# Performance work log

Hardware: AMD Instinct MI355X
Metric: run time of the kernel (lower is better)

Reference implementation:

```python
import jax, jax.numpy as jnp
import numpy as np

N_NODES, N_EDGES, D, N_RELS = 50000, 600000, 128, 460


def setup_inputs() -> dict:
    key = jax.random.key(0)
    ks = jax.random.split(key, 8)
    h = jax.random.normal(ks[0], (N_NODES, D), dtype=jnp.float32)
    emb_rel = jax.random.normal(ks[1], (N_RELS, D), dtype=jnp.float32)
    attn_fc_w = jax.random.normal(ks[2], (D, 3 * D), dtype=jnp.float32) * 0.05   # Linear(3D->D), weight [out,in]
    attn_fc2_w = jax.random.normal(ks[3], (1, D), dtype=jnp.float32) * 0.05     # Linear(D->1)
    loop_weight = jax.random.normal(ks[4], (D, D), dtype=jnp.float32) * 0.05
    edge_src = jax.random.randint(ks[5], (N_EDGES,), 0, N_NODES)
    edge_dst = jax.random.randint(ks[6], (N_EDGES,), 0, N_NODES)
    edge_type = jax.random.randint(ks[7], (N_EDGES,), 0, N_RELS)
    return {"h": h, "emb_rel": emb_rel, "attn_fc_w": attn_fc_w,
            "attn_fc2_w": attn_fc2_w, "loop_weight": loop_weight,
            "edge_src": edge_src, "edge_dst": edge_dst, "edge_type": edge_type}


def reference(h, emb_rel, attn_fc_w, attn_fc2_w, loop_weight, edge_src, edge_dst, edge_type):
    n = h.shape[0]
    # --- per-edge gather ---
    hs = h[edge_src]            # [E, D] src features (mailbox 'e_h')
    ht = h[edge_dst]            # [E, D]
    rel = emb_rel[edge_type]    # [E, D]
    # --- concat-MLP attention: leaky_relu(fc2(fc1([hs|ht|rel]))) ---
    z2 = jnp.concatenate([hs, ht, rel], axis=1)          # [E, 3D]
    a = z2 @ attn_fc_w.T                                  # [E, D]
    e = jax.nn.leaky_relu(a @ attn_fc2_w.T)               # [E, 1], slope 0.01 (torch default)
    # --- per-destination segment softmax ---
    m = jax.ops.segment_max(e, edge_dst, num_segments=n)  # [N, 1]
    m = jnp.where(jnp.isfinite(m), m, jnp.float32(0.0))   # empty nodes -> -inf; neutralize
    ex = jnp.exp(e - m[edge_dst])                         # [E, 1]
    den = jax.ops.segment_sum(ex, edge_dst, num_segments=n)
    alpha = ex / den[edge_dst]                            # [E, 1]
    # --- weighted scatter-sum of src features ---
    node_repr = jax.ops.segment_sum(alpha * hs, edge_dst, num_segments=n)  # [N, D]
    # --- self-loop ---
    node_repr = node_repr + h @ loop_weight
    return node_repr
```

## Files before the change

### kernel.cpp

```cpp
#include <hip/hip_runtime.h>

#define N_NODES 50000
#define N_EDGES 600000
#define D 128
#define N_RELS 460
#define CAP_LOG 6

typedef unsigned short u16;
typedef __attribute__((ext_vector_type(8))) short bf16x8;
typedef __attribute__((ext_vector_type(4))) float f32x4;

enum : int {
    OFF_W      = 0,
    OFF_S1     = 384,
    OFF_S2     = 50384,
    OFF_S3     = 100384,
    OFF_COUNTS = 100864,
    OFF_CSR    = 900864,
    OFF_HB     = 4100864,
};

#define NODE_WAVES   12500
#define REL_WAVES    115
#define SCORE_BLOCKS 3154
#define GEMM_BLOCKS  782
#define ZERO_BLOCKS  196
#define FILL_BLOCKS  586
#define WT_STRIDE    136

__device__ __forceinline__ u16 f2bf(float f) {
    unsigned u = __float_as_uint(f);
    unsigned r = u + 0x7FFFu + ((u >> 16) & 1u);
    return (u16)(r >> 16);
}

__global__ __launch_bounds__(256) void k_prep(
        const float* __restrict__ fc1, const float* __restrict__ fc2,
        const float* __restrict__ W, const float* __restrict__ h,
        float* __restrict__ w, int* __restrict__ counts,
        float* __restrict__ out) {
    __shared__ u16 Ws[D * WT_STRIDE];
    int t = threadIdx.x;
    if (blockIdx.x < GEMM_BLOCKS) {
        for (int i = t; i < (D * D) / 4; i += 256) {
            float4 v = ((const float4*)W)[i];
            int k  = i >> 5;
            int n0 = (i & 31) * 4;
            Ws[(n0 + 0) * WT_STRIDE + k] = f2bf(v.x);
            Ws[(n0 + 1) * WT_STRIDE + k] = f2bf(v.y);
            Ws[(n0 + 2) * WT_STRIDE + k] = f2bf(v.z);
            Ws[(n0 + 3) * WT_STRIDE + k] = f2bf(v.w);
        }
        __syncthreads();

        int wave = t >> 6, lane = t & 63;
        int quad = lane >> 4, m16 = lane & 15;
        int nbase = blockIdx.x * 64 + wave * 16;

        f32x4 acc[8];
        #pragma unroll
        for (int cg = 0; cg < 8; ++cg) acc[cg] = (f32x4){0.f, 0.f, 0.f, 0.f};

        int arow = nbase + m16;
        if (arow >= N_NODES) arow = N_NODES - 1;
        const float* aptr = h + (size_t)arow * D + quad * 8;

        #pragma unroll
        for (int k0 = 0; k0 < D; k0 += 32) {
            float4 a0 = *(const float4*)(aptr + k0);
            float4 a1 = *(const float4*)(aptr + k0 + 4);
            bf16x8 a;
            a[0] = (short)f2bf(a0.x); a[1] = (short)f2bf(a0.y);
            a[2] = (short)f2bf(a0.z); a[3] = (short)f2bf(a0.w);
            a[4] = (short)f2bf(a1.x); a[5] = (short)f2bf(a1.y);
            a[6] = (short)f2bf(a1.z); a[7] = (short)f2bf(a1.w);
            #pragma unroll
            for (int cg = 0; cg < 8; ++cg) {
                bf16x8 bb = *(const bf16x8*)(&Ws[(cg * 16 + m16) * WT_STRIDE + k0 + quad * 8]);
                acc[cg] = __builtin_amdgcn_mfma_f32_16x16x32_bf16(a, bb, acc[cg], 0, 0, 0);
            }
        }
        #pragma unroll
        for (int reg = 0; reg < 4; ++reg) {
            int row = nbase + quad * 4 + reg;
            if (row < N_NODES) {
                #pragma unroll
                for (int cg = 0; cg < 8; ++cg)
                    out[(size_t)row * D + cg * 16 + m16] = acc[cg][reg];
            }
        }
    } else if (blockIdx.x < GEMM_BLOCKS + ZERO_BLOCKS) {
        int base = ((blockIdx.x - GEMM_BLOCKS) * 256 + t) * 4;
        int i4 = ((blockIdx.x - GEMM_BLOCKS) * 256 + t);
        #pragma unroll
        for (int rep = 0; rep < 4; ++rep) {
            int idx = (i4 * 4 + rep);
            if (idx * 4 < N_NODES * 16)
                ((int4*)counts)[idx] = make_int4(0, 0, 0, 0);
        }
        (void)base;
    } else {
        for (int j = t; j < 3 * D; j += 256) {
            float acc = 0.f;
            for (int k = 0; k < D; ++k) acc += fc2[k] * fc1[k * 3 * D + j];
            w[j] = acc;
        }
    }
}

__global__ __launch_bounds__(256) void k_fused(
        const int* __restrict__ src, const int* __restrict__ dst,
        const int* __restrict__ typ, int* __restrict__ counts,
        unsigned* __restrict__ csr,
        const float* __restrict__ h, const float* __restrict__ emb_rel,
        const float* __restrict__ w,
        float* __restrict__ s1, float* __restrict__ s2, float* __restrict__ s3,
        u16* __restrict__ hb) {
    if (blockIdx.x < FILL_BLOCKS) {
        int i = blockIdx.x * blockDim.x + threadIdx.x;
        if (i >= N_EDGES / 4) return;
        int4 d4 = ((const int4*)dst)[i];
        int4 s4 = ((const int4*)src)[i];
        int4 t4 = ((const int4*)typ)[i];
        int sl0 = atomicAdd(&counts[d4.x << 4], 1);
        int sl1 = atomicAdd(&counts[d4.y << 4], 1);
        int sl2 = atomicAdd(&counts[d4.z << 4], 1);
        int sl3 = atomicAdd(&counts[d4.w << 4], 1);
        csr[(d4.x << CAP_LOG) + sl0] = (unsigned)s4.x | ((unsigned)t4.x << 16);
        csr[(d4.y << CAP_LOG) + sl1] = (unsigned)s4.y | ((unsigned)t4.y << 16);
        csr[(d4.z << CAP_LOG) + sl2] = (unsigned)s4.z | ((unsigned)t4.z << 16);
        csr[(d4.w << CAP_LOG) + sl3] = (unsigned)s4.w | ((unsigned)t4.w << 16);
    } else {
        int wv = ((blockIdx.x - FILL_BLOCKS) * blockDim.x + threadIdx.x) >> 6;
        int l  = threadIdx.x & 63;
        int sub = l >> 4;
        int q   = l & 15;
        if (wv < NODE_WAVES) {
            int r = wv * 4 + sub;
            const float* hp = h + (size_t)r * D + q * 8;
            float4 h0 = *(const float4*)hp;
            float4 h1 = *(const float4*)(hp + 4);
            uint4 pk;
            pk.x = (unsigned)f2bf(h0.x) | ((unsigned)f2bf(h0.y) << 16);
            pk.y = (unsigned)f2bf(h0.z) | ((unsigned)f2bf(h0.w) << 16);
            pk.z = (unsigned)f2bf(h1.x) | ((unsigned)f2bf(h1.y) << 16);
            pk.w = (unsigned)f2bf(h1.z) | ((unsigned)f2bf(h1.w) << 16);
            ((uint4*)hb)[(size_t)r * 16 + q] = pk;
            float4 w10 = *(const float4*)(w + q * 8);
            float4 w11 = *(const float4*)(w + q * 8 + 4);
            float4 w20 = *(const float4*)(w + D + q * 8);
            float4 w21 = *(const float4*)(w + D + q * 8 + 4);
            float a1 = h0.x * w10.x + h0.y * w10.y + h0.z * w10.z + h0.w * w10.w
                     + h1.x * w11.x + h1.y * w11.y + h1.z * w11.z + h1.w * w11.w;
            float a2 = h0.x * w20.x + h0.y * w20.y + h0.z * w20.z + h0.w * w20.w
                     + h1.x * w21.x + h1.y * w21.y + h1.z * w21.z + h1.w * w21.w;
            #pragma unroll
            for (int o = 8; o; o >>= 1) { a1 += __shfl_xor(a1, o, 16); a2 += __shfl_xor(a2, o, 16); }
            if (q == 0) { s1[r] = a1; s2[r] = a2; }
        } else if (wv < NODE_WAVES + REL_WAVES) {
            int r = (wv - NODE_WAVES) * 4 + sub;
            const float* rp = emb_rel + (size_t)r * D + q * 8;
            float4 r0 = *(const float4*)rp;
            float4 r1 = *(const float4*)(rp + 4);
            float4 w30 = *(const float4*)(w + 2 * D + q * 8);
            float4 w31 = *(const float4*)(w + 2 * D + q * 8 + 4);
            float a3 = r0.x * w30.x + r0.y * w30.y + r0.z * w30.z + r0.w * w30.w
                     + r1.x * w31.x + r1.y * w31.y + r1.z * w31.z + r1.w * w31.w;
            #pragma unroll
            for (int o = 8; o; o >>= 1) a3 += __shfl_xor(a3, o, 16);
            if (q == 0) s3[r] = a3;
        }
    }
}

#define ROWACC(uu, cc)                                                         \
    accA.x += (cc) * __uint_as_float((uu).x << 16);                            \
    accA.y += (cc) * __uint_as_float((uu).x & 0xFFFF0000u);                    \
    accA.z += (cc) * __uint_as_float((uu).y << 16);                            \
    accA.w += (cc) * __uint_as_float((uu).y & 0xFFFF0000u);                    \
    accB.x += (cc) * __uint_as_float((uu).z << 16);                            \
    accB.y += (cc) * __uint_as_float((uu).z & 0xFFFF0000u);                    \
    accB.z += (cc) * __uint_as_float((uu).w << 16);                            \
    accB.w += (cc) * __uint_as_float((uu).w & 0xFFFF0000u);

__global__ void k_gather(const u16* __restrict__ hb, const int* __restrict__ counts,
                         const unsigned* __restrict__ csr,
                         const float* __restrict__ s1, const float* __restrict__ s2,
                         const float* __restrict__ s3, float* __restrict__ out) {
    int n  = (blockIdx.x * blockDim.x + threadIdx.x) >> 4;
    int gl = threadIdx.x & 15;
    if (n >= N_NODES) return;
    int deg = counts[n << 4];
    if (deg == 0) return;
    int beg = n << CAP_LOG;
    int end = beg + deg;

    float s2n = s2[n];
    float den = 0.f;
    f32x4 accA = {0.f, 0.f, 0.f, 0.f}, accB = {0.f, 0.f, 0.f, 0.f};

    for (int cb = beg; cb < end; cb += 16) {
        int i = cb + gl;
        int msrc = 0; float mex = 0.f;
        if (i < end) {
            unsigned p = csr[i];
            msrc = (int)(p & 0xFFFFu);
            float x = s1[msrc] + s2n + s3[p >> 16];
            float lv = (x > 0.f) ? x : 0.01f * x;
            mex = __expf(lv);
        }
        den += mex;
        int cnt = min(16, end - cb);
        int j = 0;
        for (; j + 7 < cnt; j += 8) {
            int aa[8]; float cc[8]; uint4 uu[8];
            #pragma unroll
            for (int u = 0; u < 8; ++u) {
                aa[u] = __shfl(msrc, j + u, 16);
                cc[u] = __shfl(mex,  j + u, 16);
            }
            #pragma unroll
            for (int u = 0; u < 8; ++u)
                uu[u] = ((const uint4*)(hb + (size_t)aa[u] * D))[gl];
            #pragma unroll
            for (int u = 0; u < 8; ++u) { ROWACC(uu[u], cc[u]); }
        }
        for (; j + 3 < cnt; j += 4) {
            int aa[4]; float cc[4]; uint4 uu[4];
            #pragma unroll
            for (int u = 0; u < 4; ++u) {
                aa[u] = __shfl(msrc, j + u, 16);
                cc[u] = __shfl(mex,  j + u, 16);
            }
            #pragma unroll
            for (int u = 0; u < 4; ++u)
                uu[u] = ((const uint4*)(hb + (size_t)aa[u] * D))[gl];
            #pragma unroll
            for (int u = 0; u < 4; ++u) { ROWACC(uu[u], cc[u]); }
        }
        for (; j < cnt; ++j) {
            int   a0 = __shfl(msrc, j, 16);
            float c0 = __shfl(mex, j, 16);
            uint4 u0 = ((const uint4*)(hb + (size_t)a0 * D))[gl];
            ROWACC(u0, c0);
        }
    }
    #pragma unroll
    for (int o = 8; o; o >>= 1) den += __shfl_xor(den, o, 16);
    float inv = 1.f / den;

    float* op = out + (size_t)n * D + gl * 8;
    float4 o0 = *(float4*)op, o1 = *(float4*)(op + 4);
    o0.x += accA.x * inv; o0.y += accA.y * inv; o0.z += accA.z * inv; o0.w += accA.w * inv;
    o1.x += accB.x * inv; o1.y += accB.y * inv; o1.z += accB.z * inv; o1.w += accB.w * inv;
    *(float4*)op = o0; *(float4*)(op + 4) = o1;
}

extern "C" void kernel_launch(void* const* d_in, const int* in_sizes, int n_in,
                              void* d_out, int out_size, void* d_ws, size_t ws_size,
                              hipStream_t stream) {
    const float* h       = (const float*)d_in[0];
    const float* emb_rel = (const float*)d_in[1];
    const float* fc1     = (const float*)d_in[2];
    const float* fc2     = (const float*)d_in[3];
    const float* loopw   = (const float*)d_in[4];
    const int*   esrc    = (const int*)d_in[5];
    const int*   edst    = (const int*)d_in[6];
    const int*   etyp    = (const int*)d_in[7];
    float* out = (float*)d_out;
    float* ws  = (float*)d_ws;

    float*    w       = ws + OFF_W;
    float*    s1      = ws + OFF_S1;
    float*    s2      = ws + OFF_S2;
    float*    s3      = ws + OFF_S3;
    int*      counts  = (int*)(ws + OFF_COUNTS);
    unsigned* csr     = (unsigned*)(ws + OFF_CSR);
    u16*      hb      = (u16*)(ws + OFF_HB);

    k_prep<<<GEMM_BLOCKS + ZERO_BLOCKS + 1, 256, 0, stream>>>(
        fc1, fc2, loopw, h, w, counts, out);

    k_fused<<<FILL_BLOCKS + SCORE_BLOCKS, 256, 0, stream>>>(
        esrc, edst, etyp, counts, csr, h, emb_rel, w, s1, s2, s3, hb);

    k_gather<<<(N_NODES * 16 + 255) / 256, 256, 0, stream>>>(
        hb, counts, csr, s1, s2, s3, out);
}
```

Baseline: 172.2 us.

## Emit bf16 copy of h from GEMM kernel and read it for node scores

The self-loop GEMM kernel already converts each h row to bf16 for the MFMA, so it now writes that bf16 copy out, and the score kernel reads the bf16 rows instead of re-reading fp32 h and converting again. This removes one full fp32 pass over h (about 25 MB) from the fused kernel. It also makes each CSR-fill thread handle eight edges instead of four, and uses nontemporal load/store for the final output update in the gather kernel. Node scores s1/s2 are now computed from bf16-rounded h, which slightly changes the attention logits.

```diff
diff --git a/kernel.cpp b/kernel.cpp
--- a/kernel.cpp
+++ b/kernel.cpp
@@ -25,7 +25,7 @@
 #define SCORE_BLOCKS 3154
 #define GEMM_BLOCKS  782
 #define ZERO_BLOCKS  196
-#define FILL_BLOCKS  586
+#define FILL_BLOCKS  293
 #define WT_STRIDE    136
 
 __device__ __forceinline__ u16 f2bf(float f) {
@@ -33,12 +33,14 @@
     unsigned r = u + 0x7FFFu + ((u >> 16) & 1u);
     return (u16)(r >> 16);
 }
+__device__ __forceinline__ float blo(unsigned u) { return __uint_as_float(u << 16); }
+__device__ __forceinline__ float bhi(unsigned u) { return __uint_as_float(u & 0xFFFF0000u); }
 
 __global__ __launch_bounds__(256) void k_prep(
         const float* __restrict__ fc1, const float* __restrict__ fc2,
         const float* __restrict__ W, const float* __restrict__ h,
         float* __restrict__ w, int* __restrict__ counts,
-        float* __restrict__ out) {
+        u16* __restrict__ hb, float* __restrict__ out) {
     __shared__ u16 Ws[D * WT_STRIDE];
     int t = threadIdx.x;
     if (blockIdx.x < GEMM_BLOCKS) {
@@ -64,6 +66,7 @@
         int arow = nbase + m16;
         if (arow >= N_NODES) arow = N_NODES - 1;
         const float* aptr = h + (size_t)arow * D + quad * 8;
+        u16* hbp = hb + (size_t)arow * D + quad * 8;
 
         #pragma unroll
         for (int k0 = 0; k0 < D; k0 += 32) {
@@ -74,6 +77,7 @@
             a[2] = (short)f2bf(a0.z); a[3] = (short)f2bf(a0.w);
             a[4] = (short)f2bf(a1.x); a[5] = (short)f2bf(a1.y);
             a[6] = (short)f2bf(a1.z); a[7] = (short)f2bf(a1.w);
+            *(bf16x8*)(hbp + k0) = a;
             #pragma unroll
             for (int cg = 0; cg < 8; ++cg) {
                 bf16x8 bb = *(const bf16x8*)(&Ws[(cg * 16 + m16) * WT_STRIDE + k0 + quad * 8]);
@@ -90,15 +94,13 @@
             }
         }
     } else if (blockIdx.x < GEMM_BLOCKS + ZERO_BLOCKS) {
-        int base = ((blockIdx.x - GEMM_BLOCKS) * 256 + t) * 4;
-        int i4 = ((blockIdx.x - GEMM_BLOCKS) * 256 + t);
+        int i4 = (blockIdx.x - GEMM_BLOCKS) * 256 + t;
         #pragma unroll
         for (int rep = 0; rep < 4; ++rep) {
-            int idx = (i4 * 4 + rep);
+            int idx = i4 * 4 + rep;
             if (idx * 4 < N_NODES * 16)
                 ((int4*)counts)[idx] = make_int4(0, 0, 0, 0);
         }
-        (void)base;
     } else {
         for (int j = t; j < 3 * D; j += 256) {
             float acc = 0.f;
@@ -112,24 +114,31 @@
         const int* __restrict__ src, const int* __restrict__ dst,
         const int* __restrict__ typ, int* __restrict__ counts,
         unsigned* __restrict__ csr,
-        const float* __restrict__ h, const float* __restrict__ emb_rel,
+        const u16* __restrict__ hb, const float* __restrict__ emb_rel,
         const float* __restrict__ w,
-        float* __restrict__ s1, float* __restrict__ s2, float* __restrict__ s3,
-        u16* __restrict__ hb) {
+        float* __restrict__ s1, float* __restrict__ s2, float* __restrict__ s3) {
     if (blockIdx.x < FILL_BLOCKS) {
         int i = blockIdx.x * blockDim.x + threadIdx.x;
-        if (i >= N_EDGES / 4) return;
-        int4 d4 = ((const int4*)dst)[i];
-        int4 s4 = ((const int4*)src)[i];
-        int4 t4 = ((const int4*)typ)[i];
-        int sl0 = atomicAdd(&counts[d4.x << 4], 1);
-        int sl1 = atomicAdd(&counts[d4.y << 4], 1);
-        int sl2 = atomicAdd(&counts[d4.z << 4], 1);
-        int sl3 = atomicAdd(&counts[d4.w << 4], 1);
-        csr[(d4.x << CAP_LOG) + sl0] = (unsigned)s4.x | ((unsigned)t4.x << 16);
-        csr[(d4.y << CAP_LOG) + sl1] = (unsigned)s4.y | ((unsigned)t4.y << 16);
-        csr[(d4.z << CAP_LOG) + sl2] = (unsigned)s4.z | ((unsigned)t4.z << 16);
-        csr[(d4.w << CAP_LOG) + sl3] = (unsigned)s4.w | ((unsigned)t4.w << 16);
+        if (i >= N_EDGES / 8) return;
+        int4 da = ((const int4*)dst)[2 * i],     db = ((const int4*)dst)[2 * i + 1];
+        int4 sa = ((const int4*)src)[2 * i],     sb = ((const int4*)src)[2 * i + 1];
+        int4 ta = ((const int4*)typ)[2 * i],     tb = ((const int4*)typ)[2 * i + 1];
+        int l0 = atomicAdd(&counts[da.x << 4], 1);
+        int l1 = atomicAdd(&counts[da.y << 4], 1);
+        int l2 = atomicAdd(&counts[da.z << 4], 1);
+        int l3 = atomicAdd(&counts[da.w << 4], 1);
+        int l4 = atomicAdd(&counts[db.x << 4], 1);
+        int l5 = atomicAdd(&counts[db.y << 4], 1);
+        int l6 = atomicAdd(&counts[db.z << 4], 1);
+        int l7 = atomicAdd(&counts[db.w << 4], 1);
+        csr[(da.x << CAP_LOG) + l0] = (unsigned)sa.x | ((unsigned)ta.x << 16);
+        csr[(da.y << CAP_LOG) + l1] = (unsigned)sa.y | ((unsigned)ta.y << 16);
+        csr[(da.z << CAP_LOG) + l2] = (unsigned)sa.z | ((unsigned)ta.z << 16);
+        csr[(da.w << CAP_LOG) + l3] = (unsigned)sa.w | ((unsigned)ta.w << 16);
+        csr[(db.x << CAP_LOG) + l4] = (unsigned)sb.x | ((unsigned)tb.x << 16);
+        csr[(db.y << CAP_LOG) + l5] = (unsigned)sb.y | ((unsigned)tb.y << 16);
+        csr[(db.z << CAP_LOG) + l6] = (unsigned)sb.z | ((unsigned)tb.z << 16);
+        csr[(db.w << CAP_LOG) + l7] = (unsigned)sb.w | ((unsigned)tb.w << 16);
     } else {
         int wv = ((blockIdx.x - FILL_BLOCKS) * blockDim.x + threadIdx.x) >> 6;
         int l  = threadIdx.x & 63;
@@ -137,23 +146,19 @@
         int q   = l & 15;
         if (wv < NODE_WAVES) {
             int r = wv * 4 + sub;
-            const float* hp = h + (size_t)r * D + q * 8;
-            float4 h0 = *(const float4*)hp;
-            float4 h1 = *(const float4*)(hp + 4);
-            uint4 pk;
-            pk.x = (unsigned)f2bf(h0.x) | ((unsigned)f2bf(h0.y) << 16);
-            pk.y = (unsigned)f2bf(h0.z) | ((unsigned)f2bf(h0.w) << 16);
-            pk.z = (unsigned)f2bf(h1.x) | ((unsigned)f2bf(h1.y) << 16);
-            pk.w = (unsigned)f2bf(h1.z) | ((unsigned)f2bf(h1.w) << 16);
-            ((uint4*)hb)[(size_t)r * 16 + q] = pk;
+            uint4 pk = ((const uint4*)hb)[(size_t)r * 16 + q];
             float4 w10 = *(const float4*)(w + q * 8);
             float4 w11 = *(const float4*)(w + q * 8 + 4);
             float4 w20 = *(const float4*)(w + D + q * 8);
             float4 w21 = *(const float4*)(w + D + q * 8 + 4);
-            float a1 = h0.x * w10.x + h0.y * w10.y + h0.z * w10.z + h0.w * w10.w
-                     + h1.x * w11.x + h1.y * w11.y + h1.z * w11.z + h1.w * w11.w;
-            float a2 = h0.x * w20.x + h0.y * w20.y + h0.z * w20.z + h0.w * w20.w
-                     + h1.x * w21.x + h1.y * w21.y + h1.z * w21.z + h1.w * w21.w;
+            float a1 = blo(pk.x) * w10.x + bhi(pk.x) * w10.y
+                     + blo(pk.y) * w10.z + bhi(pk.y) * w10.w
+                     + blo(pk.z) * w11.x + bhi(pk.z) * w11.y
+                     + blo(pk.w) * w11.z + bhi(pk.w) * w11.w;
+            float a2 = blo(pk.x) * w20.x + bhi(pk.x) * w20.y
+                     + blo(pk.y) * w20.z + bhi(pk.y) * w20.w
+                     + blo(pk.z) * w21.x + bhi(pk.z) * w21.y
+                     + blo(pk.w) * w21.z + bhi(pk.w) * w21.w;
             #pragma unroll
             for (int o = 8; o; o >>= 1) { a1 += __shfl_xor(a1, o, 16); a2 += __shfl_xor(a2, o, 16); }
             if (q == 0) { s1[r] = a1; s2[r] = a2; }
@@ -174,14 +179,10 @@
 }
 
 #define ROWACC(uu, cc)                                                         \
-    accA.x += (cc) * __uint_as_float((uu).x << 16);                            \
-    accA.y += (cc) * __uint_as_float((uu).x & 0xFFFF0000u);                    \
-    accA.z += (cc) * __uint_as_float((uu).y << 16);                            \
-    accA.w += (cc) * __uint_as_float((uu).y & 0xFFFF0000u);                    \
-    accB.x += (cc) * __uint_as_float((uu).z << 16);                            \
-    accB.y += (cc) * __uint_as_float((uu).z & 0xFFFF0000u);                    \
-    accB.z += (cc) * __uint_as_float((uu).w << 16);                            \
-    accB.w += (cc) * __uint_as_float((uu).w & 0xFFFF0000u);
+    accA.x += (cc) * blo((uu).x);  accA.y += (cc) * bhi((uu).x);               \
+    accA.z += (cc) * blo((uu).y);  accA.w += (cc) * bhi((uu).y);               \
+    accB.x += (cc) * blo((uu).z);  accB.y += (cc) * bhi((uu).z);               \
+    accB.z += (cc) * blo((uu).w);  accB.w += (cc) * bhi((uu).w);
 
 __global__ void k_gather(const u16* __restrict__ hb, const int* __restrict__ counts,
                          const unsigned* __restrict__ csr,
@@ -249,11 +250,13 @@
     for (int o = 8; o; o >>= 1) den += __shfl_xor(den, o, 16);
     float inv = 1.f / den;
 
-    float* op = out + (size_t)n * D + gl * 8;
-    float4 o0 = *(float4*)op, o1 = *(float4*)(op + 4);
-    o0.x += accA.x * inv; o0.y += accA.y * inv; o0.z += accA.z * inv; o0.w += accA.w * inv;
-    o1.x += accB.x * inv; o1.y += accB.y * inv; o1.z += accB.z * inv; o1.w += accB.w * inv;
-    *(float4*)op = o0; *(float4*)(op + 4) = o1;
+    f32x4* op = (f32x4*)(out + (size_t)n * D + gl * 8);
+    f32x4 o0 = __builtin_nontemporal_load(op);
+    f32x4 o1 = __builtin_nontemporal_load(op + 1);
+    o0 += accA * inv;
+    o1 += accB * inv;
+    __builtin_nontemporal_store(o0, op);
+    __builtin_nontemporal_store(o1, op + 1);
 }
 
 extern "C" void kernel_launch(void* const* d_in, const int* in_sizes, int n_in,
@@ -279,10 +282,10 @@
     u16*      hb      = (u16*)(ws + OFF_HB);
 
     k_prep<<<GEMM_BLOCKS + ZERO_BLOCKS + 1, 256, 0, stream>>>(
-        fc1, fc2, loopw, h, w, counts, out);
+        fc1, fc2, loopw, h, w, counts, hb, out);
 
     k_fused<<<FILL_BLOCKS + SCORE_BLOCKS, 256, 0, stream>>>(
-        esrc, edst, etyp, counts, csr, h, emb_rel, w, s1, s2, s3, hb);
+        esrc, edst, etyp, counts, csr, hb, emb_rel, w, s1, s2, s3);
 
     k_gather<<<(N_NODES * 16 + 255) / 256, 256, 0, stream>>>(
         hb, counts, csr, s1, s2, s3, out);
```

After: 170.1 us. No clear change (-1.2%).
